# Performance work log

Measured on AMD Instinct MI355X. Metric: run time of the kernel, lower is better.

## Reference

```python
import jax, jax.numpy as jnp
import numpy as np


def conv3d(x, w, b, stride=(1, 1, 1)):
    # x: (B,C,D,H,W), w: (O,I,3,3,3), padding 1 on all three dims (PyTorch Conv3d k=3,p=1)
    y = jax.lax.conv_general_dilated(
        x, w, stride, [(1, 1)] * 3,
        dimension_numbers=("NCDHW", "OIDHW", "NCDHW"))
    return y + b[None, :, None, None, None]


def deconv3d(x, w, b):
    # ConvTranspose3d with k=3, s=1, p=1 == conv with spatially flipped kernel
    return conv3d(x, jnp.flip(w, axis=(2, 3, 4)), b)


def upsample2x(x):
    # nn.Upsample(scale_factor=(1,2,2), mode='nearest')
    return jnp.repeat(jnp.repeat(x, 2, axis=3), 2, axis=4)


def fo_pool(z, f, reverse):
    # linear gated recurrence h_t = f_t*h_{t-1} + (1-f_t)*z_t along band axis (dim 2)
    zt = jnp.moveaxis(z, 2, 0)
    ft = jnp.moveaxis(f, 2, 0)
    if reverse:
        zt, ft = zt[::-1], ft[::-1]

    def step(h, zf):
        zi, fi = zf
        h = fi * h + (1.0 - fi) * zi
        return h, h

    _, hs = jax.lax.scan(step, jnp.zeros_like(zt[0]), (zt, ft))
    if reverse:
        hs = hs[::-1]
    return jnp.moveaxis(hs, 0, 2)


def qrnn(gates, reverse):
    z, f = jnp.split(gates, 2, axis=1)
    return fo_pool(jnp.tanh(z), jax.nn.sigmoid(f), reverse)


def biqrnn(gates):
    z, f1, f2 = jnp.split(gates, 3, axis=1)
    z = jnp.tanh(z)
    return (fo_pool(z, jax.nn.sigmoid(f1), False)
            + fo_pool(z, jax.nn.sigmoid(f2), True))


def _forward(x, fe_w, fe_b, e0_w, e0_b, e1_w, e1_b, e2_w, e2_b, e3_w, e3_b,
             e4_w, e4_b, d0_w, d0_b, d1_w, d1_b, d2_w, d2_b, d3_w, d3_b,
             d4_w, d4_b, rec_w, rec_b):
    # feature extractor: BiQRNNConv3D(1 -> 16), gates 48ch
    fe = biqrnn(conv3d(x, fe_w, fe_b))                        # (B,16,31,256,256)
    # encoder (alternating direction: F,T,F,T,F)
    e0 = qrnn(conv3d(fe, e0_w, e0_b), False)                  # 16ch @256
    e1 = qrnn(conv3d(e0, e1_w, e1_b, stride=(1, 2, 2)), True) # 32ch @128
    e2 = qrnn(conv3d(e1, e2_w, e2_b), False)                  # 32ch @128
    e3 = qrnn(conv3d(e2, e3_w, e3_b, stride=(1, 2, 2)), True) # 64ch @64
    e4 = qrnn(conv3d(e3, e4_w, e4_b), False)                  # 64ch @64
    # decoder (reverse starts at True after encoder toggles)
    d0 = qrnn(deconv3d(e4, d0_w, d0_b), True)                 # 64ch @64
    d1 = qrnn(conv3d(upsample2x(d0 + e3), d1_w, d1_b), False) # 32ch @128
    d2 = qrnn(deconv3d(d1 + e2, d2_w, d2_b), True)            # 32ch @128
    d3 = qrnn(conv3d(upsample2x(d2 + e1), d3_w, d3_b), False) # 16ch @256
    d4 = qrnn(deconv3d(d3 + e0, d4_w, d4_b), True)            # 16ch @256
    out = d4 + fe
    # reconstructor: BiQRNNDeConv3D(16 -> 1), act='tanh'
    out = biqrnn(deconv3d(out, rec_w, rec_b))                 # (B,1,31,256,256)
    return out + x


def setup_inputs() -> dict:
    key = jax.random.key(0)
    ks = jax.random.split(key, 26)

    def W(k, o, i):
        return jax.random.normal(k, (o, i, 3, 3, 3), jnp.float32) * 0.05

    def Bv(k, o):
        return jax.random.normal(k, (o,), jnp.float32) * 0.01

    x = jax.random.normal(ks[0], (1, 1, 31, 256, 256), jnp.float32)
    inp = {"x": x}
    shapes = {
        "fe": (48, 1), "e0": (32, 16), "e1": (64, 16), "e2": (64, 32),
        "e3": (128, 32), "e4": (128, 64), "d0": (128, 64), "d1": (64, 64),
        "d2": (64, 32), "d3": (32, 32), "d4": (32, 16), "rec": (3, 16),
    }
    for j, (name, (o, i)) in enumerate(shapes.items()):
        inp[name + "_w"] = W(ks[1 + 2 * j], o, i)
        inp[name + "_b"] = Bv(ks[2 + 2 * j], o)
    return inp


def reference(x, fe_w, fe_b, e0_w, e0_b, e1_w, e1_b, e2_w, e2_b, e3_w, e3_b,
              e4_w, e4_b, d0_w, d0_b, d1_w, d1_b, d2_w, d2_b, d3_w, d3_b,
              d4_w, d4_b, rec_w, rec_b):
    return _forward(x, fe_w, fe_b, e0_w, e0_b, e1_w, e1_b, e2_w, e2_b,
                    e3_w, e3_b, e4_w, e4_b, d0_w, d0_b, d1_w, d1_b,
                    d2_w, d2_b, d3_w, d3_b, d4_w, d4_b, rec_w, rec_b)
```

## Files before the change

### kernel.cpp

```cpp
#include <hip/hip_runtime.h>
#include <hip/hip_bf16.h>
#include <cstdint>
#include <cstddef>

using f16 = _Float16;
typedef _Float16 f16x2 __attribute__((ext_vector_type(2)));
typedef _Float16 f16x8 __attribute__((ext_vector_type(8)));
typedef float f32x4 __attribute__((ext_vector_type(4)));

static constexpr int DD = 31;
static constexpr long long U  = 31LL * 256 * 256;
static constexpr long long V2 = 31LL * 128 * 128;
static constexpr long long POOL_UNITS = 56;
static constexpr int CP_CHUNK = 16;
static constexpr int COSPLIT_NONE = 1 << 30;

union U32H2 { unsigned u; f16x2 h; };

__device__ __forceinline__ float toF(float v) { return v; }
__device__ __forceinline__ float toF(f16 v) { return (float)v; }
__device__ __forceinline__ void stv(float* p, float v) { *p = v; }
__device__ __forceinline__ void stv(f16* p, float v) { *p = (f16)v; }
__device__ __forceinline__ float sigm(float x) { return 1.f / (1.f + __expf(-x)); }

// ... 24 lines not shown
    for (long long i = (long long)blockIdx.x * 256 + threadIdx.x; i < n; i += stride)
        p[i] = (f16)0.f;
}

__global__ __launch_bounds__(256)
void add_k(f16* __restrict__ a, const f16* __restrict__ b, long long n8)
{
    const long long i = (long long)blockIdx.x * 256 + threadIdx.x;
    if (i >= n8) return;
    uint4 va = ((const uint4*)a)[i];
    const uint4 vb = ((const uint4*)b)[i];
    va.x = addh2(va.x, vb.x); va.y = addh2(va.y, vb.y);
    va.z = addh2(va.z, vb.z); va.w = addh2(va.w, vb.w);
    ((uint4*)a)[i] = va;
}

__global__ __launch_bounds__(256)
void pack_w_k(const float* __restrict__ wt, f16* __restrict__ outp,
              int CIN, int nCo, int flip)
{
    const int e = blockIdx.x * 256 + threadIdx.x;
    const int nhg = (nCo + 7) >> 3;
    const int total = (CIN >> 3) * nhg * 9 * 64;
    if (e >= total) return;
    const int l = e & 63;
    const int r = e >> 6;
    const int r9 = r % 9;
    const int t2 = r / 9;
    const int hg = t2 % nhg;
    const int cc = t2 / nhg;
    const int kd = r9 / 3, Tg = r9 - kd * 3;
    const int n = hg * 8 + (l & 15);
    const int T = Tg * 4 + (l >> 4);
    f16x8 bv;
#pragma unroll
    for (int i = 0; i < 8; ++i) bv[i] = (f16)0.f;
    if (T <= 8 && n < nCo) {
        const int kh = T / 3, kw = T - (T / 3) * 3;
        const int st = flip ? ((2 - kd) * 9 + (2 - kh) * 3 + (2 - kw))
                            : (kd * 9 + kh * 3 + kw);
        const size_t wb8 = ((size_t)n * CIN + cc * 8) * 27 + st;
#pragma unroll
        for (int i = 0; i < 8; ++i)
            bv[i] = (f16)wt[wb8 + (size_t)i * 27];
    }
    *(f16x8*)(outp + (size_t)e * 8) = bv;
}

template<int STRIDE, bool FLIP, int CIN, int HOUT, int WOUT, int NT, bool PACKED,
         bool OUTIL>
__global__ __launch_bounds__(256)
void conv_mfma_k(const f16* __restrict__ in, const float* __restrict__ wt,
                 const f16x8* __restrict__ wb, const float* __restrict__ bias,
                 f16* __restrict__ out, f16* __restrict__ outF, int coSplit,
                 int nCo, int cg0, int nhg)
{
    constexpr int CIC = CIN / 8;
    constexpr int HIN = HOUT * STRIDE, WIN = WOUT * STRIDE;
    constexpr int WT = (WOUT > 128) ? 128 : WOUT;
    constexpr int RR = 128 / WT;
    constexpr int COLS = WOUT / WT;
    constexpr int TPD = (HOUT / RR) * COLS;
    constexpr int AH = STRIDE * (RR - 1) + 3;
    constexpr int AW = STRIDE * (WT - 1) + 3;
    constexpr int APOS = 3 * AH * AW;
    constexpr int NBENT = NT * 576;

    extern __shared__ unsigned lds[];
    unsigned* Alds = lds;
    unsigned* Blds = lds + APOS * 4;

    const int tid = threadIdx.x;
    const int l = tid & 63;
    const int wid = tid >> 6;

    const int bx = blockIdx.x;
    const int d0 = bx / TPD;
    const int rem = bx - d0 * TPD;
    const int h0 = (rem / COLS) * RR;
    const int wb_ = (rem % COLS) * WT;

    const int co_base = blockIdx.y * (16 * NT);
    const int nRem = nCo - co_base;
    const int hgBase = cg0 + blockIdx.y * (2 * NT);

    const int base_h = STRIDE * h0 - 1;
    const int base_w = STRIDE * wb_ - 1;
    constexpr size_t HWin = (size_t)HIN * WIN;
    constexpr size_t DHW = (size_t)DD * HWin;
    const unsigned* inu = (const unsigned*)in;

    int hho[2], wlo[2];
#pragma unroll
    for (int mt = 0; mt < 2; ++mt) {
        const int p = wid * 32 + mt * 16 + (l & 15);
        hho[mt] = p / WT;
        wlo[mt] = p - hho[mt] * WT;
    }
    const int g = l >> 4;
    int khg[3], kwg[3];
#pragma unroll
    for (int Tg = 0; Tg < 3; ++Tg) {
        int T = Tg * 4 + g;
        if (T > 8) T = 8;
        khg[Tg] = T / 3;
        kwg[Tg] = T - (T / 3) * 3;
    }
// ... 49 lines not shown
                const int T = Tg * 4 + gg;
                f16x8 bv;
                if (T <= 8 && n < nRem) {
                    const int kh = T / 3, kw = T - (T / 3) * 3;
                    const int st = FLIP ? ((2 - kd) * 9 + (2 - kh) * 3 + (2 - kw))
                                        : (kd * 9 + kh * 3 + kw);
                    const size_t wb8 = ((size_t)(co_base + n) * CIN + cc * 8) * 27 + st;
#pragma unroll
                    for (int e = 0; e < 8; ++e)
                        bv[e] = (f16)wt[wb8 + (size_t)e * 27];
                } else {
#pragma unroll
                    for (int e = 0; e < 8; ++e) bv[e] = (f16)0.f;
                }
                *(f16x8*)(Blds + (size_t)t * 4) = bv;
            }
        }
        __syncthreads();
#pragma unroll
        for (int kd = 0; kd < 3; ++kd) {
#pragma unroll
            for (int Tg = 0; Tg < 3; ++Tg) {
                f16x8 bfrag[NT];
#pragma unroll
                for (int nt = 0; nt < NT; ++nt)
                    bfrag[nt] = PACKED ? bfr[nt][kd * 3 + Tg]
                                       : *(const f16x8*)
                        (Blds + (size_t)(((nt * 9) + kd * 3 + Tg) * 64 + l) * 4);
                const int kh = khg[Tg], kw = kwg[Tg];
#pragma unroll
                for (int mt = 0; mt < 2; ++mt) {
                    const int hh = STRIDE * hho[mt] + kh;
                    const int ww = STRIDE * wlo[mt] + kw;
                    const f16x8 afrag = *(const f16x8*)
                        (Alds + (size_t)((kd * AH + hh) * AW + ww) * 4);
#pragma unroll
                    for (int nt = 0; nt < NT; ++nt)
                        acc[mt][nt] = __builtin_amdgcn_mfma_f32_16x16x32_f16(
                            afrag, bfrag[nt], acc[mt][nt], 0, 0, 0);
                }
            }
        }
    }

    const int n = l & 15;
#pragma unroll
    for (int nt = 0; nt < NT; ++nt) {
        const int ng = nt * 16 + n;
        if (ng < nRem) {
            const int co = co_base + ng;
            const float bv = bias[co];
            f16* dst = out;
            int cs = co;
            if (OUTIL && co >= coSplit) { dst = outF; cs = co - coSplit; }
#pragma unroll
            for (int mt = 0; mt < 2; ++mt) {
#pragma unroll
                for (int r = 0; r < 4; ++r) {
                    const int p = wid * 32 + mt * 16 + (l >> 4) * 4 + r;
                    const int hh = p / WT;
                    const int wl = p - hh * WT;
                    const int h = h0 + hh, w = wb_ + wl;
                    const float val = acc[mt][nt][r] + bv;
                    if (OUTIL) {
                        const size_t coPlane =
                            (size_t)(cs >> 1) * DD * HOUT * WOUT * 2 + (cs & 1);
                        dst[coPlane + ((size_t)d0 * HOUT + h) * WOUT * 2 +
                            (size_t)w * 2] = (f16)val;
                    } else {
                        out[((size_t)co * DD + d0) * HOUT * WOUT +
                            (size_t)h * WOUT + w] = (f16)val;
                    }
                }
            }
        }
    }
}

template<int CIN, int HLO, int WLO, int NT>
__global__ __launch_bounds__(256)
void conv_mfma_up_k(const f16* __restrict__ in, const f16x8* __restrict__ wb,
                    const float* __restrict__ bias, f16* __restrict__ out,
                    f16* __restrict__ outF, int coSplit,
                    int nCo, int cg0, int nhg)
{
    constexpr int CIC = CIN / 8;
    constexpr int HOUT = 2 * HLO, WOUT = 2 * WLO;
    constexpr int WT = (WOUT > 128) ? 128 : WOUT;
    constexpr int COLS = WOUT / WT;
    constexpr int TPD = HOUT * COLS;
    constexpr int AWLO = WT / 2 + 2;
    constexpr int AWLOP = AWLO + 1;
    constexpr int APOS = 3 * 2 * AWLO;

    extern __shared__ unsigned lds[];

    const int tid = threadIdx.x;
    const int l = tid & 63;
    const int wid = tid >> 6;

    const int bx = blockIdx.x;
    const int d0 = bx / TPD;
    const int rem = bx - d0 * TPD;
    const int h0 = rem / COLS;
    const int wb_ = (rem % COLS) * WT;

    const int co_base = blockIdx.y * (16 * NT);
    const int nRem = nCo - co_base;
    const int hgBase = cg0 + blockIdx.y * (2 * NT);

    const int rlo0 = (h0 - 1) >> 1;
    const int clo0 = (wb_ >> 1) - 1;

    constexpr size_t HWlo = (size_t)HLO * WLO;
    constexpr size_t DHW = (size_t)DD * HWlo;
    const unsigned* inu = (const unsigned*)in;

    int wpos[2];
#pragma unroll
    for (int mt = 0; mt < 2; ++mt)
        wpos[mt] = wid * 32 + mt * 16 + (l & 15);

    const int g = l >> 4;
    int khg[3], kwg[3];
#pragma unroll
    for (int Tg = 0; Tg < 3; ++Tg) {
        int T = Tg * 4 + g;
        if (T > 8) T = 8;
        khg[Tg] = T / 3;
        kwg[Tg] = T - (T / 3) * 3;
    }

    f32x4 acc[2][NT];
#pragma unroll
    for (int mt = 0; mt < 2; ++mt)
#pragma unroll
        for (int nt = 0; nt < NT; ++nt)
            acc[mt][nt] = (f32x4){0.f, 0.f, 0.f, 0.f};

    for (int cc = 0; cc < CIC; ++cc) {
        f16x8 bfr[NT][9];
#pragma unroll
        for (int nt = 0; nt < NT; ++nt)
#pragma unroll
            for (int r9 = 0; r9 < 9; ++r9)
                bfr[nt][r9] = wb[((size_t)cc * nhg + hgBase + nt * 2) * 9 * 64
                                 + (size_t)r9 * 64 + l];
        __syncthreads();
        for (int t = tid; t < APOS; t += 256) {
            const int ww = t % AWLO;
            const int t2 = t / AWLO;
            const int rr = t2 & 1;
            const int dd = t2 >> 1;
            const int d = d0 - 1 + dd;
            const int hlo = rlo0 + rr;
            const int wlo = clo0 + ww;
            uint4 val = make_uint4(0u, 0u, 0u, 0u);
            if ((unsigned)d < (unsigned)DD && (unsigned)hlo < (unsigned)HLO &&
                (unsigned)wlo < (unsigned)WLO) {
                const size_t gi = (size_t)(cc * 4) * DHW +
                                  (size_t)d * HWlo + (size_t)hlo * WLO + wlo;
                val.x = inu[gi];
                val.y = inu[gi + DHW];
                val.z = inu[gi + 2 * DHW];
                val.w = inu[gi + 3 * DHW];
            }
            *(uint4*)(lds + (size_t)((dd * 2 + rr) * AWLOP + ww) * 4) = val;
        }
        __syncthreads();
#pragma unroll
        for (int kd = 0; kd < 3; ++kd) {
#pragma unroll
            for (int Tg = 0; Tg < 3; ++Tg) {
                const int kh = khg[Tg], kw = kwg[Tg];
                const int rr = ((h0 + kh - 1) >> 1) - rlo0;
#pragma unroll
                for (int mt = 0; mt < 2; ++mt) {
                    const int iw = ((wpos[mt] + kw - 1) >> 1) + 1;
                    const f16x8 afrag = *(const f16x8*)
                        (lds + (size_t)((kd * 2 + rr) * AWLOP + iw) * 4);
#pragma unroll
                    for (int nt = 0; nt < NT; ++nt)
                        acc[mt][nt] = __builtin_amdgcn_mfma_f32_16x16x32_f16(
                            afrag, bfr[nt][kd * 3 + Tg], acc[mt][nt], 0, 0, 0);
                }
            }
        }
    }

    const int n = l & 15;
#pragma unroll
    for (int nt = 0; nt < NT; ++nt) {
        const int ng = nt * 16 + n;
        if (ng < nRem) {
            const int co = co_base + ng;
            const float bv = bias[co];
            f16* dst = out;
            int cs = co;
            if (co >= coSplit) { dst = outF; cs = co - coSplit; }
            const size_t coPlane = (size_t)(cs >> 1) * DD * HOUT * WOUT * 2 + (cs & 1);
#pragma unroll
            for (int mt = 0; mt < 2; ++mt) {
#pragma unroll
                for (int r = 0; r < 4; ++r) {
                    const int p = wid * 32 + mt * 16 + (l >> 4) * 4 + r;
                    dst[coPlane + ((size_t)d0 * HOUT + h0) * WOUT * 2 +
                        (size_t)(wb_ + p) * 2] = (f16)(acc[mt][nt][r] + bv);
                }
            }
        }
    }
}

template<int STRIDE, bool FLIP, int CO_BLK, bool OUT_IL>
__global__ __launch_bounds__(256, 2)
void conv3d_il_k(const f16* __restrict__ in, const float* __restrict__ wt,
                 const float* __restrict__ bias, f16* __restrict__ out,
                 int Cin, int Hin, int Win, int Hout, int Wout)
{
    extern __shared__ unsigned wl2[];
    const int co_base = blockIdx.y * CO_BLK;

    const int s8 = (blockIdx.x * 256 + threadIdx.x) * 8;
    const int w0 = s8 % Wout;
    const int sh = s8 / Wout;
    const int h0 = sh % Hout;
    const int d0 = sh / Hout;

    float acc[CO_BLK][8];
#pragma unroll
    for (int j = 0; j < CO_BLK; ++j) {
        const float bv = bias[co_base + j];
#pragma unroll
        for (int o = 0; o < 8; ++o) acc[j][o] = bv;
    }

    const size_t HWin = (size_t)Hin * Win;
    const int CP = Cin >> 1;

    for (int cp0 = 0; cp0 < CP; cp0 += CP_CHUNK) {
        const int cnp = (CP - cp0 < CP_CHUNK) ? (CP - cp0) : CP_CHUNK;
        __syncthreads();
        for (int t = threadIdx.x; t < cnp * 27 * CO_BLK; t += 256) {
            const int j = t % CO_BLK;
            const int k = (t / CO_BLK) % 27;
            const int cp = t / (CO_BLK * 27);
            int src;
            if (FLIP) {
                const int kd = k / 9, kh = (k / 3) % 3, kw = k % 3;
                src = (2 - kd) * 9 + (2 - kh) * 3 + (2 - kw);
            } else {
                src = k;
// ... 260 lines not shown
    const long long idx = (long long)blockIdx.x * 256 + threadIdx.x;
    if (idx >= (long long)C * HW) return;
    size_t base; size_t step;
    if (IL) {
        const long long pairIdx = idx / (2LL * HW);
        const int rem = (int)(idx - pairIdx * 2LL * HW);
        const int p = rem >> 1;
        const int par = rem & 1;
        base = ((size_t)pairIdx * DD * HW + p) * 2 + par;
        step = (size_t)HW * 2;
    } else {
        const int c = (int)(idx / HW);
        const int p = (int)(idx - (long long)c * HW);
        base = (size_t)c * DD * HW + p;
        step = (size_t)HW;
    }
    float h = 0.f;
    if (!reverse) {
        for (int d = 0; d < DD; ++d) {
            const size_t off = base + (size_t)d * step;
            const float zz = tanhf(toF(z[off]));
            const float ff = sigm(toF(f[off]));
            h = ff * h + (1.f - ff) * zz;
            float v = h;
            if (a1) v += toF(a1[off]);
            if (a2) v += toF(a2[off]);
            stv(out + off, v);
        }
    } else {
        for (int d = DD - 1; d >= 0; --d) {
            const size_t off = base + (size_t)d * step;
            const float zz = tanhf(toF(z[off]));
            const float ff = sigm(toF(f[off]));
            h = ff * h + (1.f - ff) * zz;
            float v = h;
            if (a1) v += toF(a1[off]);
            if (a2) v += toF(a2[off]);
            stv(out + off, v);
        }
    }
}

__global__ __launch_bounds__(256)
void diag_k(float* out, float v, int n)
{
    const int i = blockIdx.x * 256 + threadIdx.x;
    if (i < n) out[i] = v;
}


template<int STRIDE, bool FLIP, int CIN, int HOUT, int WOUT, int NT, bool PACKED,
         bool OUTIL>
static inline void mfma_launch(const f16* in, const float* w, const f16x8* wb,
                               const float* b, f16* out, f16* outF, int coSplit,
                               int co0, int nCo, int nhg, hipStream_t s)
{
    constexpr int WT = WOUT > 128 ? 128 : WOUT;
    constexpr int RR = 128 / WT;
    constexpr int AH = STRIDE * (RR - 1) + 3;
    constexpr int AW = STRIDE * (WT - 1) + 3;
    constexpr size_t lds = (size_t)(3 * AH * AW) * 16 +
                           (PACKED ? 0 : (size_t)NT * 9216);
    dim3 grid((unsigned)(DD * (HOUT / RR) * (WOUT / WT)),
              (unsigned)((nCo + 16 * NT - 1) / (16 * NT)));
    conv_mfma_k<STRIDE, FLIP, CIN, HOUT, WOUT, NT, PACKED, OUTIL>
        <<<grid, 256, lds, s>>>(
        in, w + (size_t)co0 * CIN * 27, wb, b + co0, out, outF, coSplit,
        nCo, co0 / 8, nhg);
}

template<int CIN, int HLO, int WLO, int NT>
static inline void mfma_up_launch(const f16* in, const f16x8* wb,
                                  const float* b, f16* out, f16* outF,
                                  int coSplit, int co0, int nCo,
                                  int nhg, hipStream_t s)
{
    constexpr int WOUT = 2 * WLO;
    constexpr int WT = WOUT > 128 ? 128 : WOUT;
    constexpr int AWLOP = WT / 2 + 3;
    constexpr size_t lds = (size_t)(3 * 2 * AWLOP) * 16;
    dim3 grid((unsigned)(DD * (2 * HLO) * (WOUT / WT)),
              (unsigned)((nCo + 16 * NT - 1) / (16 * NT)));
    conv_mfma_up_k<CIN, HLO, WLO, NT><<<grid, 256, lds, s>>>(
        in, wb, b + co0, out, outF, coSplit, nCo, co0 / 8, nhg);
}

static inline void conv_launch(const f16* in, const float* w, const float* b,
                               f16* out, int Cin, int co0, int nCo,
                               int Hin, int Win, int Hout, int Wout,
                               int stride, bool flip, hipStream_t s)
{
    const unsigned gx = (unsigned)((DD * (long long)Hout * Wout) / 2048);
    const float* wp = w + (size_t)co0 * Cin * 27;
    const float* bp = b + co0;
    const int cpc = (Cin / 2 < CP_CHUNK) ? Cin / 2 : CP_CHUNK;
    if (flip) {
        if (nCo % 4 == 0) {
            dim3 grid(gx, nCo / 4);
            conv3d_il_k<1, true, 4, true><<<grid, 256, (size_t)cpc * 27 * 4 * 4, s>>>(
                in, wp, bp, out, Cin, Hin, Win, Hout, Wout);
        } else {
            dim3 grid(gx, 1);
            conv3d_il_k<1, true, 3, false><<<grid, 256, (size_t)cpc * 27 * 3 * 4, s>>>(
                in, wp, bp, out, Cin, Hin, Win, Hout, Wout);
        }
    } else {
        dim3 grid(gx, nCo / 8);
        conv3d_il_k<1, false, 8, true><<<grid, 256, (size_t)cpc * 27 * 8 * 4, s>>>(
            in, wp, bp, out, Cin, Hin, Win, Hout, Wout);
    }
}

static inline void conv_up_launch(const f16* ia, const f16* ib, const float* w,
                                  const float* b, f16* out, int Cin, int co0,
                                  int nCo, int Hlo, int Wlo, hipStream_t s)
{
    const unsigned gx = (unsigned)((DD * 4LL * Hlo * Wlo) / 2048);
    const int cpc = (Cin / 2 < CP_CHUNK) ? Cin / 2 : CP_CHUNK;
    if (nCo % 8 == 0) {
        dim3 grid(gx, nCo / 8);
        conv3d_up_il_k<8><<<grid, 256, (size_t)cpc * 27 * 8 * 4, s>>>(
            ia, ib, w + (size_t)co0 * Cin * 27, b + co0, out, Cin, Hlo, Wlo);
    } else {
        dim3 grid(gx, nCo / 4);
        conv3d_up_il_k<4><<<grid, 256, (size_t)cpc * 27 * 4 * 4, s>>>(
            ia, ib, w + (size_t)co0 * Cin * 27, b + co0, out, Cin, Hlo, Wlo);
    }
}

template<bool IL, typename TA1, typename TA2, typename TO>
static inline void pool_launch(const f16* z, const f16* f, TO* o, const TA1* a1,
                               const TA2* a2, int C, int HW, int rev,
                               hipStream_t s)
{
    const long long tot = (long long)C * HW;
    fo_pool_k<IL, TA1, TA2, TO><<<(unsigned)((tot + 255) / 256), 256, 0, s>>>(
        z, f, o, a1, a2, C, HW, rev);
}

static inline void pack_launch(const float* w, f16* outp, int CIN, int nCo,
                               int flip, hipStream_t s)
{
    const int total = (CIN / 8) * ((nCo + 7) / 8) * 9 * 64;
    pack_w_k<<<(total + 255) / 256, 256, 0, s>>>(w, outp, CIN, nCo, flip);
}

static inline void add_launch(f16* a, const f16* b, long long n, hipStream_t s)
{
    const long long n8 = n / 8;
    add_k<<<(unsigned)((n8 + 255) / 256), 256, 0, s>>>(a, b, n8);
}

static constexpr size_t pk_sz(int CIN, int nCo)
{ return (size_t)(CIN / 8) * ((nCo + 7) / 8) * 9 * 64 * 8; }

static void run_net(const float* x, const float* const* W, const float* const* B,
                    float* out, f16* P, bool packed, hipStream_t s)
{
    const f16* np = nullptr;
    const float* npf = nullptr;

    f16* WP = P + 56 * U;
    f16* PK_e0 = WP;
    f16* PK_e1 = PK_e0 + pk_sz(16, 32);
    f16* PK_e2 = PK_e1 + pk_sz(16, 64);
    f16* PK_e3 = PK_e2 + pk_sz(32, 64);
    f16* PK_e4 = PK_e3 + pk_sz(32, 128);
    f16* PK_d0 = PK_e4 + pk_sz(64, 128);
    f16* PK_d2 = PK_d0 + pk_sz(64, 128);
    f16* PK_d1 = PK_d0;
    f16* PK_d3 = PK_d1 + pk_sz(64, 64);
    f16* PK_d4 = PK_d3 + pk_sz(32, 32);
    f16* PK_rec = PK_d4 + pk_sz(16, 32);
    if (packed) {
        pack_launch(W[1], PK_e0, 16, 32, 0, s);
        pack_launch(W[2], PK_e1, 16, 64, 0, s);
        pack_launch(W[3], PK_e2, 32, 64, 0, s);
        pack_launch(W[4], PK_e3, 32, 128, 0, s);
        pack_launch(W[5], PK_e4, 64, 128, 0, s);
        pack_launch(W[6], PK_d0, 64, 128, 1, s);
        pack_launch(W[8], PK_d2, 32, 64, 1, s);
    }

#define MFMA_CALL(S, F, CI, H, Wd, NTv, in_, wt_, wb_, bi_, out_, co0_, nco_, nhg_) \
    do { if (packed) mfma_launch<S, F, CI, H, Wd, NTv, true, true>(in_, wt_, (const f16x8*)(wb_), bi_, out_, nullptr, COSPLIT_NONE, co0_, nco_, nhg_, s); \
         else        mfma_launch<S, F, CI, H, Wd, NTv, false, true>(in_, wt_, nullptr, bi_, out_, nullptr, COSPLIT_NONE, co0_, nco_, nhg_, s); } while (0)

    fill_k<<<2048, 256, 0, s>>>(P, POOL_UNITS * U);

    f16* FE = P + 32 * U;
    for (int a = 0; a < 16; a += 4) {
        conv_fe_k<<<992, 256, 0, s>>>(x, W[0] + (size_t)a * 27,        B[0] + a,      P);
        conv_fe_k<<<992, 256, 0, s>>>(x, W[0] + (size_t)(16 + a) * 27, B[0] + 16 + a, P + 4 * U);
        conv_fe_k<<<992, 256, 0, s>>>(x, W[0] + (size_t)(32 + a) * 27, B[0] + 32 + a, P + 8 * U);
        pool_launch<true, f16, float, f16>(P, P + 4 * U, P + 12 * U, np, npf, 4, 65536, 0, s);
        pool_launch<true, f16, float, f16>(P, P + 8 * U, FE + (size_t)a * U, P + 12 * U, npf, 4, 65536, 1, s);
    }

    f16* E0 = P + 16 * U;
    if (packed) {
        f16* G = P + 48 * U;
        mfma_launch<1, false, 16, 256, 256, 2, true, true>(
            FE, W[1], (const f16x8*)PK_e0, B[1], P, G, 16, 0, 24, 4, s);
        pool_launch<true, f16, float, f16>(P, G, E0, np, npf, 8, 65536, 0, s);
        mfma_launch<1, false, 16, 256, 256, 1, true, true>(
            FE, W[1], (const f16x8*)PK_e0, B[1], G, nullptr, COSPLIT_NONE,
            24, 8, 4, s);
        pool_launch<true, f16, float, f16>(P + 8 * U, G, E0 + 8 * U, np, npf, 8, 65536, 0, s);
    } else {
        MFMA_CALL(1, false, 16, 256, 256, 1, FE, W[1], PK_e0, B[1], P, 0, 16, 4);
        for (int a = 0; a < 16; a += 8) {
            f16* G = P + 48 * U;
            MFMA_CALL(1, false, 16, 256, 256, 1, FE, W[1], PK_e0, B[1], G, 16 + a, 8, 4);
            pool_launch<true, f16, float, f16>(P + (size_t)a * U, G, E0 + (size_t)a * U,
                                               np, npf, 8, 65536, 0, s);
        }
    }

    f16* E1 = P;
    {
        f16* G = P + 32 * U;
        MFMA_CALL(2, false, 16, 128, 128, 2, E0, W[2], PK_e1, B[2], G, 0, 64, 8);
        pool_launch<true, f16, float, f16>(G, G + 8 * U, E1, np, npf, 32, 16384, 1, s);
    }

    f16* E2 = P + 8 * U;
    {
        f16* G = P + 32 * U;
        MFMA_CALL(1, false, 32, 128, 128, 2, E1, W[3], PK_e2, B[3], G, 0, 64, 8);
        pool_launch<true, f16, float, f16>(G, G + 8 * U, E2, np, npf, 32, 16384, 0, s);
    }

    f16* E3 = P + 32 * U;
    {
        f16* G = P + 48 * U;
        MFMA_CALL(2, false, 32, 64, 64, 2, E2, W[4], PK_e3, B[4], G, 0, 128, 16);
        pool_launch<true, f16, float, f16>(G, G + 4 * U, E3, np, npf, 64, 4096, 1, s);
    }

    f16* E4 = P + 40 * U;
    {
        f16* G = P + 48 * U;
        MFMA_CALL(1, false, 64, 64, 64, 2, E3, W[5], PK_e4, B[5], G, 0, 128, 16);
        pool_launch<true, f16, float, f16>(G, G + 4 * U, E4, np, npf, 64, 4096, 0, s);
    }

    f16* D0 = P + 44 * U;
    {
        f16* G = P + 48 * U;
        MFMA_CALL(1, true, 64, 64, 64, 2, E4, W[6], PK_d0, B[6], G, 0, 128, 16);
        pool_launch<true, f16, float, f16>(G, G + 4 * U, D0, np, npf, 64, 4096, 1, s);
    }
    if (packed) {
        pack_launch(W[7],  PK_d1, 64, 64, 0, s);
        pack_launch(W[9],  PK_d3, 32, 32, 0, s);
        pack_launch(W[10], PK_d4, 16, 32, 1, s);
        pack_launch(W[11], PK_rec, 16, 3, 1, s);
    }

    f16* D1 = P + 36 * U;
    if (packed)
        add_launch(D0, E3, 4 * U, s);
    for (int a = 0; a < 32; a += 16) {
        f16* G = P + 48 * U;
        if (packed) {
            mfma_up_launch<64, 64, 64, 1>(D0, (const f16x8*)PK_d1, B[7], G,
                                          nullptr, COSPLIT_NONE, a, 16, 8, s);
            mfma_up_launch<64, 64, 64, 1>(D0, (const f16x8*)PK_d1, B[7], G + 4 * U,
                                          nullptr, COSPLIT_NONE, 32 + a, 16, 8, s);
        } else {
            conv_up_launch(D0, E3, W[7], B[7], G,         64, a,      16, 64, 64, s);
            conv_up_launch(D0, E3, W[7], B[7], G + 4 * U, 64, 32 + a, 16, 64, 64, s);
        }
        pool_launch<true, f16, float, f16>(G, G + 4 * U, D1 + (size_t)a * V2,
                                           E2 + (size_t)a * V2, npf, 16, 16384, 0, s);
    }

    f16* D2 = P + 8 * U;
    for (int a = 0; a < 32; a += 16) {
        f16* G = P + 48 * U;
        MFMA_CALL(1, true, 32, 128, 128, 1, D1, W[8], PK_d2, B[8], G,         a,      16, 8);
        MFMA_CALL(1, true, 32, 128, 128, 1, D1, W[8], PK_d2, B[8], G + 4 * U, 32 + a, 16, 8);
        pool_launch<true, f16, float, f16>(G, G + 4 * U, D2 + (size_t)a * V2, np, npf, 16, 16384, 1, s);
    }

    f16* D3 = P + 32 * U;
    if (packed) {
        f16* G = P + 48 * U;
        add_launch(D2, E1, 8 * U, s);
        mfma_up_launch<32, 128, 128, 2>(D2, (const f16x8*)PK_d3, B[9], D3,
                                        G, 16, 0, 24, 4, s);
        pool_launch<true, f16, float, f16>(D3, G, D3, E0, npf, 8, 65536, 0, s);
        mfma_up_launch<32, 128, 128, 1>(D2, (const f16x8*)PK_d3, B[9], G,
                                        nullptr, COSPLIT_NONE, 24, 8, 4, s);
        pool_launch<true, f16, float, f16>(D3 + 8 * U, G, D3 + 8 * U,
                                           E0 + 8 * U, npf, 8, 65536, 0, s);
    } else {
        for (int a = 0; a < 16; a += 4) {
            f16* G = P + 48 * U;
            conv_up_launch(D2, E1, W[9], B[9], G,         32, a,      4, 128, 128, s);
            conv_up_launch(D2, E1, W[9], B[9], G + 4 * U, 32, 16 + a, 4, 128, 128, s);
            pool_launch<true, f16, float, f16>(G, G + 4 * U, D3 + (size_t)a * U,
                                               E0 + (size_t)a * U, npf, 4, 65536, 0, s);
        }
    }

    f16* FE2 = P;
    for (int a = 0; a < 16; a += 4) {
        f16* G = P + 16 * U;
        conv_fe_k<<<992, 256, 0, s>>>(x, W[0] + (size_t)a * 27,        B[0] + a,      G);
        conv_fe_k<<<992, 256, 0, s>>>(x, W[0] + (size_t)(16 + a) * 27, B[0] + 16 + a, G + 4 * U);
        conv_fe_k<<<992, 256, 0, s>>>(x, W[0] + (size_t)(32 + a) * 27, B[0] + 32 + a, G + 8 * U);
        pool_launch<true, f16, float, f16>(G, G + 4 * U, G + 12 * U, np, npf, 4, 65536, 0, s);
        pool_launch<true, f16, float, f16>(G, G + 8 * U, FE2 + (size_t)a * U, G + 12 * U, npf, 4, 65536, 1, s);
    }

    f16* D4 = P + 16 * U;
    if (packed) {
        f16* G = P + 48 * U;
        mfma_launch<1, true, 16, 256, 256, 2, true, true>(
            D3, W[10], (const f16x8*)PK_d4, B[10], D4, G, 16, 0, 24, 4, s);
        pool_launch<true, f16, float, f16>(D4, G, D4, FE2, npf, 8, 65536, 1, s);
        mfma_launch<1, true, 16, 256, 256, 1, true, true>(
            D3, W[10], (const f16x8*)PK_d4, B[10], G, nullptr, COSPLIT_NONE,
            24, 8, 4, s);
        pool_launch<true, f16, float, f16>(D4 + 8 * U, G, D4 + 8 * U,
                                           FE2 + 8 * U, npf, 8, 65536, 1, s);
    } else {
        for (int a = 0; a < 16; a += 4) {
            f16* G = P + 48 * U;
            conv_launch(D3, W[10], B[10], G,         16, a,      4, 256, 256, 256, 256, 1, true, s);
            conv_launch(D3, W[10], B[10], G + 4 * U, 16, 16 + a, 4, 256, 256, 256, 256, 1, true, s);
            pool_launch<true, f16, float, f16>(G, G + 4 * U, D4 + (size_t)a * U,
                                               FE2 + (size_t)a * U, npf, 4, 65536, 1, s);
        }
    }

    {
        f16* G = P + 32 * U;
        f16* TMP = P + 35 * U;
        if (packed) {
            mfma_launch<1, true, 16, 256, 256, 1, true, false>(
                D4, W[11], (const f16x8*)PK_rec, B[11], G, nullptr, COSPLIT_NONE,
                0, 3, 1, s);
        } else {
            conv_launch(D4, W[11], B[11], G, 16, 0, 3, 256, 256, 256, 256, 1, true, s);
        }
        pool_launch<false, f16, float, f16>(G, G + 1 * U, TMP, np, npf, 1, 65536, 0, s);
        pool_launch<false, f16, float, float>(G, G + 2 * U, out, TMP, x, 1, 65536, 1, s);
    }
#undef MFMA_CALL
}

extern "C" void kernel_launch(void* const* d_in, const int* in_sizes, int n_in,
                              void* d_out, int out_size, void* d_ws, size_t ws_size,
                              hipStream_t stream)
{
    const float* x = (const float*)d_in[0];
    const float* W[12];
    const float* B[12];
    for (int i = 0; i < 12; ++i) {
        W[i] = (const float*)d_in[1 + 2 * i];
        B[i] = (const float*)d_in[2 + 2 * i];
    }

    const size_t need_base = (size_t)(POOL_UNITS * U) * sizeof(f16);
    const size_t need_pack = (size_t)(57 * U) * sizeof(f16);
    if (ws_size >= need_pack) {
        run_net(x, W, B, (float*)d_out, (f16*)d_ws, true, stream);
    } else if (ws_size >= need_base) {
        run_net(x, W, B, (float*)d_out, (f16*)d_ws, false, stream);
    } else {
        const float ws_mb = (float)((double)ws_size / 1048576.0);
        diag_k<<<(out_size + 255) / 256, 256, 0, stream>>>(
            (float*)d_out, ws_mb, out_size);
    }
}
```

Baseline: 4.282 ms.

## Stage upsampled input in LDS at full resolution and merge d1 conv launches

The upsample-conv kernel now writes the nearest-upsampled input tile into LDS at output resolution (WT+2 columns), duplicating each low-res pixel. A-fragment reads then become a contiguous index wpos+kw with no shift arithmetic, and neighbouring lanes hit distinct addresses instead of duplicated ones. The d1 stage uses NT=2 with two 32-channel launches writing z directly into D1, followed by a single in-place pool, replacing four launches and two pools. The cost is roughly twice the LDS footprint and global-load work per tile, plus higher register pressure from NT=2.

```diff
diff --git a/kernel.cpp b/kernel.cpp
--- a/kernel.cpp
+++ b/kernel.cpp
@@ -293,9 +293,8 @@
     constexpr int WT = (WOUT > 128) ? 128 : WOUT;
     constexpr int COLS = WOUT / WT;
     constexpr int TPD = HOUT * COLS;
-    constexpr int AWLO = WT / 2 + 2;
-    constexpr int AWLOP = AWLO + 1;
-    constexpr int APOS = 3 * 2 * AWLO;
+    constexpr int AWHI = WT + 2;
+    constexpr int APOS = 3 * 2 * AWHI;
 
     extern __shared__ unsigned lds[];
 
@@ -314,7 +313,6 @@
     const int hgBase = cg0 + blockIdx.y * (2 * NT);
 
     const int rlo0 = (h0 - 1) >> 1;
-    const int clo0 = (wb_ >> 1) - 1;
 
     constexpr size_t HWlo = (size_t)HLO * WLO;
     constexpr size_t DHW = (size_t)DD * HWlo;
@@ -352,13 +350,13 @@
                                  + (size_t)r9 * 64 + l];
         __syncthreads();
         for (int t = tid; t < APOS; t += 256) {
-            const int ww = t % AWLO;
-            const int t2 = t / AWLO;
+            const int ww = t % AWHI;
+            const int t2 = t / AWHI;
             const int rr = t2 & 1;
             const int dd = t2 >> 1;
             const int d = d0 - 1 + dd;
             const int hlo = rlo0 + rr;
-            const int wlo = clo0 + ww;
+            const int wlo = (wb_ - 1 + ww) >> 1;
             uint4 val = make_uint4(0u, 0u, 0u, 0u);
             if ((unsigned)d < (unsigned)DD && (unsigned)hlo < (unsigned)HLO &&
                 (unsigned)wlo < (unsigned)WLO) {
@@ -369,7 +367,7 @@
                 val.z = inu[gi + 2 * DHW];
                 val.w = inu[gi + 3 * DHW];
             }
-            *(uint4*)(lds + (size_t)((dd * 2 + rr) * AWLOP + ww) * 4) = val;
+            *(uint4*)(lds + (size_t)((dd * 2 + rr) * AWHI + ww) * 4) = val;
         }
         __syncthreads();
 #pragma unroll
@@ -380,9 +378,9 @@
                 const int rr = ((h0 + kh - 1) >> 1) - rlo0;
 #pragma unroll
                 for (int mt = 0; mt < 2; ++mt) {
-                    const int iw = ((wpos[mt] + kw - 1) >> 1) + 1;
+                    const int iw = wpos[mt] + kw;
                     const f16x8 afrag = *(const f16x8*)
-                        (lds + (size_t)((kd * 2 + rr) * AWLOP + iw) * 4);
+                        (lds + (size_t)((kd * 2 + rr) * AWHI + iw) * 4);
 #pragma unroll
                     for (int nt = 0; nt < NT; ++nt)
                         acc[mt][nt] = __builtin_amdgcn_mfma_f32_16x16x32_f16(
@@ -793,8 +791,8 @@
 {
     constexpr int WOUT = 2 * WLO;
     constexpr int WT = WOUT > 128 ? 128 : WOUT;
-    constexpr int AWLOP = WT / 2 + 3;
-    constexpr size_t lds = (size_t)(3 * 2 * AWLOP) * 16;
+    constexpr int AWHI = WT + 2;
+    constexpr size_t lds = (size_t)(3 * 2 * AWHI) * 16;
     dim3 grid((unsigned)(DD * (2 * HLO) * (WOUT / WT)),
               (unsigned)((nCo + 16 * NT - 1) / (16 * NT)));
     conv_mfma_up_k<CIN, HLO, WLO, NT><<<grid, 256, lds, s>>>(
@@ -975,21 +973,22 @@
     }
 
     f16* D1 = P + 36 * U;
-    if (packed)
+    if (packed) {
+        f16* G = P + 48 * U;
         add_launch(D0, E3, 4 * U, s);
-    for (int a = 0; a < 32; a += 16) {
-        f16* G = P + 48 * U;
-        if (packed) {
-            mfma_up_launch<64, 64, 64, 1>(D0, (const f16x8*)PK_d1, B[7], G,
-                                          nullptr, COSPLIT_NONE, a, 16, 8, s);
-            mfma_up_launch<64, 64, 64, 1>(D0, (const f16x8*)PK_d1, B[7], G + 4 * U,
-                                          nullptr, COSPLIT_NONE, 32 + a, 16, 8, s);
-        } else {
+        mfma_up_launch<64, 64, 64, 2>(D0, (const f16x8*)PK_d1, B[7], D1,
+                                      nullptr, COSPLIT_NONE, 0, 32, 8, s);
+        mfma_up_launch<64, 64, 64, 2>(D0, (const f16x8*)PK_d1, B[7], G,
+                                      nullptr, COSPLIT_NONE, 32, 32, 8, s);
+        pool_launch<true, f16, float, f16>(D1, G, D1, E2, npf, 32, 16384, 0, s);
+    } else {
+        for (int a = 0; a < 32; a += 16) {
+            f16* G = P + 48 * U;
             conv_up_launch(D0, E3, W[7], B[7], G,         64, a,      16, 64, 64, s);
             conv_up_launch(D0, E3, W[7], B[7], G + 4 * U, 64, 32 + a, 16, 64, 64, s);
-        }
-        pool_launch<true, f16, float, f16>(G, G + 4 * U, D1 + (size_t)a * V2,
-                                           E2 + (size_t)a * V2, npf, 16, 16384, 0, s);
+            pool_launch<true, f16, float, f16>(G, G + 4 * U, D1 + (size_t)a * V2,
+                                               E2 + (size_t)a * V2, npf, 16, 16384, 0, s);
+        }
     }
 
     f16* D2 = P + 8 * U;
```

Measured after the change: 4.302 ms. About the same (+0.5%).

## Keep feature-extractor output in spare workspace and merge decoder channel-chunk launches

Applied to the files above, without the earlier changes.

When the workspace is large enough, the feature-extractor output is written to a dedicated region past the packed weights. The decoder then reuses it instead of recomputing the conv and bidirectional pool a second time. The d1 and d2 stages also drop their two-iteration channel loops in favour of one wider launch per gate half (NT=2, 32 channels) with a single pool over all channels, cutting launch count. In exchange the workspace must hold more memory, and the whole saving depends on the harness providing that space.

```diff
diff --git a/kernel.cpp b/kernel.cpp
--- a/kernel.cpp
+++ b/kernel.cpp
@@ -871,7 +871,7 @@
 { return (size_t)(CIN / 8) * ((nCo + 7) / 8) * 9 * 64 * 8; }
 
 static void run_net(const float* x, const float* const* W, const float* const* B,
-                    float* out, f16* P, bool packed, hipStream_t s)
+                    float* out, f16* P, bool packed, bool saveFE, hipStream_t s)
 {
     const f16* np = nullptr;
     const float* npf = nullptr;
@@ -904,7 +904,7 @@
 
     fill_k<<<2048, 256, 0, s>>>(P, POOL_UNITS * U);
 
-    f16* FE = P + 32 * U;
+    f16* FE = saveFE ? (P + 57 * U) : (P + 32 * U);
     for (int a = 0; a < 16; a += 4) {
         conv_fe_k<<<992, 256, 0, s>>>(x, W[0] + (size_t)a * 27,        B[0] + a,      P);
         conv_fe_k<<<992, 256, 0, s>>>(x, W[0] + (size_t)(16 + a) * 27, B[0] + 16 + a, P + 4 * U);
@@ -975,29 +975,37 @@
     }
 
     f16* D1 = P + 36 * U;
-    if (packed)
+    if (packed) {
+        f16* G = P + 48 * U;
         add_launch(D0, E3, 4 * U, s);
-    for (int a = 0; a < 32; a += 16) {
-        f16* G = P + 48 * U;
-        if (packed) {
-            mfma_up_launch<64, 64, 64, 1>(D0, (const f16x8*)PK_d1, B[7], G,
-                                          nullptr, COSPLIT_NONE, a, 16, 8, s);
-            mfma_up_launch<64, 64, 64, 1>(D0, (const f16x8*)PK_d1, B[7], G + 4 * U,
-                                          nullptr, COSPLIT_NONE, 32 + a, 16, 8, s);
-        } else {
+        mfma_up_launch<64, 64, 64, 2>(D0, (const f16x8*)PK_d1, B[7], D1,
+                                      nullptr, COSPLIT_NONE, 0, 32, 8, s);
+        mfma_up_launch<64, 64, 64, 2>(D0, (const f16x8*)PK_d1, B[7], G,
+                                      nullptr, COSPLIT_NONE, 32, 32, 8, s);
+        pool_launch<true, f16, float, f16>(D1, G, D1, E2, npf, 32, 16384, 0, s);
+    } else {
+        for (int a = 0; a < 32; a += 16) {
+            f16* G = P + 48 * U;
             conv_up_launch(D0, E3, W[7], B[7], G,         64, a,      16, 64, 64, s);
             conv_up_launch(D0, E3, W[7], B[7], G + 4 * U, 64, 32 + a, 16, 64, 64, s);
-        }
-        pool_launch<true, f16, float, f16>(G, G + 4 * U, D1 + (size_t)a * V2,
-                                           E2 + (size_t)a * V2, npf, 16, 16384, 0, s);
+            pool_launch<true, f16, float, f16>(G, G + 4 * U, D1 + (size_t)a * V2,
+                                               E2 + (size_t)a * V2, npf, 16, 16384, 0, s);
+        }
     }
 
     f16* D2 = P + 8 * U;
-    for (int a = 0; a < 32; a += 16) {
+    if (packed) {
         f16* G = P + 48 * U;
-        MFMA_CALL(1, true, 32, 128, 128, 1, D1, W[8], PK_d2, B[8], G,         a,      16, 8);
-        MFMA_CALL(1, true, 32, 128, 128, 1, D1, W[8], PK_d2, B[8], G + 4 * U, 32 + a, 16, 8);
-        pool_launch<true, f16, float, f16>(G, G + 4 * U, D2 + (size_t)a * V2, np, npf, 16, 16384, 1, s);
+        MFMA_CALL(1, true, 32, 128, 128, 2, D1, W[8], PK_d2, B[8], D2, 0, 32, 8);
+        MFMA_CALL(1, true, 32, 128, 128, 2, D1, W[8], PK_d2, B[8], G, 32, 32, 8);
+        pool_launch<true, f16, float, f16>(D2, G, D2, np, npf, 32, 16384, 1, s);
+    } else {
+        for (int a = 0; a < 32; a += 16) {
+            f16* G = P + 48 * U;
+            MFMA_CALL(1, true, 32, 128, 128, 1, D1, W[8], PK_d2, B[8], G,         a,      16, 8);
+            MFMA_CALL(1, true, 32, 128, 128, 1, D1, W[8], PK_d2, B[8], G + 4 * U, 32 + a, 16, 8);
+            pool_launch<true, f16, float, f16>(G, G + 4 * U, D2 + (size_t)a * V2, np, npf, 16, 16384, 1, s);
+        }
     }
 
     f16* D3 = P + 32 * U;
@@ -1021,14 +1029,19 @@
         }
     }
 
-    f16* FE2 = P;
-    for (int a = 0; a < 16; a += 4) {
-        f16* G = P + 16 * U;
-        conv_fe_k<<<992, 256, 0, s>>>(x, W[0] + (size_t)a * 27,        B[0] + a,      G);
-        conv_fe_k<<<992, 256, 0, s>>>(x, W[0] + (size_t)(16 + a) * 27, B[0] + 16 + a, G + 4 * U);
-        conv_fe_k<<<992, 256, 0, s>>>(x, W[0] + (size_t)(32 + a) * 27, B[0] + 32 + a, G + 8 * U);
-        pool_launch<true, f16, float, f16>(G, G + 4 * U, G + 12 * U, np, npf, 4, 65536, 0, s);
-        pool_launch<true, f16, float, f16>(G, G + 8 * U, FE2 + (size_t)a * U, G + 12 * U, npf, 4, 65536, 1, s);
+    f16* FE2;
+    if (saveFE) {
+        FE2 = FE;
+    } else {
+        FE2 = P;
+        for (int a = 0; a < 16; a += 4) {
+            f16* G = P + 16 * U;
+            conv_fe_k<<<992, 256, 0, s>>>(x, W[0] + (size_t)a * 27,        B[0] + a,      G);
+            conv_fe_k<<<992, 256, 0, s>>>(x, W[0] + (size_t)(16 + a) * 27, B[0] + 16 + a, G + 4 * U);
+            conv_fe_k<<<992, 256, 0, s>>>(x, W[0] + (size_t)(32 + a) * 27, B[0] + 32 + a, G + 8 * U);
+            pool_launch<true, f16, float, f16>(G, G + 4 * U, G + 12 * U, np, npf, 4, 65536, 0, s);
+            pool_launch<true, f16, float, f16>(G, G + 8 * U, FE2 + (size_t)a * U, G + 12 * U, npf, 4, 65536, 1, s);
+        }
     }
 
     f16* D4 = P + 16 * U;
@@ -1082,10 +1095,12 @@
 
     const size_t need_base = (size_t)(POOL_UNITS * U) * sizeof(f16);
     const size_t need_pack = (size_t)(57 * U) * sizeof(f16);
+    const size_t need_save = (size_t)(74 * U) * sizeof(f16);
     if (ws_size >= need_pack) {
-        run_net(x, W, B, (float*)d_out, (f16*)d_ws, true, stream);
+        const bool saveFE = (ws_size >= need_save);
+        run_net(x, W, B, (float*)d_out, (f16*)d_ws, true, saveFE, stream);
     } else if (ws_size >= need_base) {
-        run_net(x, W, B, (float*)d_out, (f16*)d_ws, false, stream);
+        run_net(x, W, B, (float*)d_out, (f16*)d_ws, false, false, stream);
     } else {
         const float ws_mb = (float)((double)ws_size / 1048576.0);
         diag_k<<<(out_size + 255) / 256, 256, 0, stream>>>(
```

Result: faster. 4.040 ms (-5.7%).

## Merge split conv launches into single wide-NT launches with dual output split

Applied to the files above, without the earlier changes.

Adds a second output pointer and split threshold to the MFMA conv kernels so one launch can write its z/f gate channels to separate buffers. Several layers (e0, d1, d2, d3) that were split into multiple conv+pool launches are merged into one conv launch followed by one pool launch. The channel tile NT rises from 2 to 4 for the 128- and 64-resolution layers, so each block covers more output channels and reuses its staged input more. The costs are more accumulator registers per thread, possibly lower occupancy, and larger scratch buffers live at once.

```diff
diff --git a/kernel.cpp b/kernel.cpp
--- a/kernel.cpp
+++ b/kernel.cpp
@@ -100,7 +100,8 @@
 __global__ __launch_bounds__(256)
 void conv_mfma_k(const f16* __restrict__ in, const float* __restrict__ wt,
                  const f16x8* __restrict__ wb, const float* __restrict__ bias,
-                 f16* __restrict__ out, f16* __restrict__ outF, int coSplit,
+                 f16* __restrict__ out, f16* __restrict__ outF,
+                 f16* __restrict__ outF2, int coSplit, int coSplit2,
                  int nCo, int cg0, int nhg)
 {
     constexpr int CIC = CIN / 8;
@@ -256,7 +257,8 @@
             const float bv = bias[co];
             f16* dst = out;
             int cs = co;
-            if (OUTIL && co >= coSplit) { dst = outF; cs = co - coSplit; }
+            if (OUTIL && co >= coSplit2) { dst = outF2; cs = co - coSplit2; }
+            else if (OUTIL && co >= coSplit) { dst = outF; cs = co - coSplit; }
 #pragma unroll
             for (int mt = 0; mt < 2; ++mt) {
 #pragma unroll
@@ -285,8 +287,8 @@
 __global__ __launch_bounds__(256)
 void conv_mfma_up_k(const f16* __restrict__ in, const f16x8* __restrict__ wb,
                     const float* __restrict__ bias, f16* __restrict__ out,
-                    f16* __restrict__ outF, int coSplit,
-                    int nCo, int cg0, int nhg)
+                    f16* __restrict__ outF, f16* __restrict__ outF2,
+                    int coSplit, int coSplit2, int nCo, int cg0, int nhg)
 {
     constexpr int CIC = CIN / 8;
     constexpr int HOUT = 2 * HLO, WOUT = 2 * WLO;
@@ -401,7 +403,8 @@
             const float bv = bias[co];
             f16* dst = out;
             int cs = co;
-            if (co >= coSplit) { dst = outF; cs = co - coSplit; }
+            if (co >= coSplit2) { dst = outF2; cs = co - coSplit2; }
+            else if (co >= coSplit) { dst = outF; cs = co - coSplit; }
             const size_t coPlane = (size_t)(cs >> 1) * DD * HOUT * WOUT * 2 + (cs & 1);
 #pragma unroll
             for (int mt = 0; mt < 2; ++mt) {
@@ -768,7 +771,8 @@
 template<int STRIDE, bool FLIP, int CIN, int HOUT, int WOUT, int NT, bool PACKED,
          bool OUTIL>
 static inline void mfma_launch(const f16* in, const float* w, const f16x8* wb,
-                               const float* b, f16* out, f16* outF, int coSplit,
+                               const float* b, f16* out, f16* outF, f16* outF2,
+                               int coSplit, int coSplit2,
                                int co0, int nCo, int nhg, hipStream_t s)
 {
     constexpr int WT = WOUT > 128 ? 128 : WOUT;
@@ -781,15 +785,15 @@
               (unsigned)((nCo + 16 * NT - 1) / (16 * NT)));
     conv_mfma_k<STRIDE, FLIP, CIN, HOUT, WOUT, NT, PACKED, OUTIL>
         <<<grid, 256, lds, s>>>(
-        in, w + (size_t)co0 * CIN * 27, wb, b + co0, out, outF, coSplit,
-        nCo, co0 / 8, nhg);
+        in, w + (size_t)co0 * CIN * 27, wb, b + co0, out, outF, outF2,
+        coSplit, coSplit2, nCo, co0 / 8, nhg);
 }
 
 template<int CIN, int HLO, int WLO, int NT>
 static inline void mfma_up_launch(const f16* in, const f16x8* wb,
                                   const float* b, f16* out, f16* outF,
-                                  int coSplit, int co0, int nCo,
-                                  int nhg, hipStream_t s)
+                                  f16* outF2, int coSplit, int coSplit2,
+                                  int co0, int nCo, int nhg, hipStream_t s)
 {
     constexpr int WOUT = 2 * WLO;
     constexpr int WT = WOUT > 128 ? 128 : WOUT;
@@ -798,7 +802,7 @@
     dim3 grid((unsigned)(DD * (2 * HLO) * (WOUT / WT)),
               (unsigned)((nCo + 16 * NT - 1) / (16 * NT)));
     conv_mfma_up_k<CIN, HLO, WLO, NT><<<grid, 256, lds, s>>>(
-        in, wb, b + co0, out, outF, coSplit, nCo, co0 / 8, nhg);
+        in, wb, b + co0, out, outF, outF2, coSplit, coSplit2, nCo, co0 / 8, nhg);
 }
 
 static inline void conv_launch(const f16* in, const float* w, const float* b,
@@ -875,6 +879,7 @@
 {
     const f16* np = nullptr;
     const float* npf = nullptr;
+    f16* NPF16 = nullptr;
 
     f16* WP = P + 56 * U;
     f16* PK_e0 = WP;
@@ -899,8 +904,8 @@
     }
 
 #define MFMA_CALL(S, F, CI, H, Wd, NTv, in_, wt_, wb_, bi_, out_, co0_, nco_, nhg_) \
-    do { if (packed) mfma_launch<S, F, CI, H, Wd, NTv, true, true>(in_, wt_, (const f16x8*)(wb_), bi_, out_, nullptr, COSPLIT_NONE, co0_, nco_, nhg_, s); \
-         else        mfma_launch<S, F, CI, H, Wd, NTv, false, true>(in_, wt_, nullptr, bi_, out_, nullptr, COSPLIT_NONE, co0_, nco_, nhg_, s); } while (0)
+    do { if (packed) mfma_launch<S, F, CI, H, Wd, NTv, true, true>(in_, wt_, (const f16x8*)(wb_), bi_, out_, NPF16, NPF16, COSPLIT_NONE, COSPLIT_NONE, co0_, nco_, nhg_, s); \
+         else        mfma_launch<S, F, CI, H, Wd, NTv, false, true>(in_, wt_, nullptr, bi_, out_, NPF16, NPF16, COSPLIT_NONE, COSPLIT_NONE, co0_, nco_, nhg_, s); } while (0)
 
     fill_k<<<2048, 256, 0, s>>>(P, POOL_UNITS * U);
 
@@ -915,14 +920,10 @@
 
     f16* E0 = P + 16 * U;
     if (packed) {
-        f16* G = P + 48 * U;
         mfma_launch<1, false, 16, 256, 256, 2, true, true>(
-            FE, W[1], (const f16x8*)PK_e0, B[1], P, G, 16, 0, 24, 4, s);
-        pool_launch<true, f16, float, f16>(P, G, E0, np, npf, 8, 65536, 0, s);
-        mfma_launch<1, false, 16, 256, 256, 1, true, true>(
-            FE, W[1], (const f16x8*)PK_e0, B[1], G, nullptr, COSPLIT_NONE,
-            24, 8, 4, s);
-        pool_launch<true, f16, float, f16>(P + 8 * U, G, E0 + 8 * U, np, npf, 8, 65536, 0, s);
+            FE, W[1], (const f16x8*)PK_e0, B[1], P, E0, NPF16,
+            16, COSPLIT_NONE, 0, 32, 4, s);
+        pool_launch<true, f16, float, f16>(P, E0, E0, np, npf, 16, 65536, 0, s);
     } else {
         MFMA_CALL(1, false, 16, 256, 256, 1, FE, W[1], PK_e0, B[1], P, 0, 16, 4);
         for (int a = 0; a < 16; a += 8) {
@@ -936,35 +937,35 @@
     f16* E1 = P;
     {
         f16* G = P + 32 * U;
-        MFMA_CALL(2, false, 16, 128, 128, 2, E0, W[2], PK_e1, B[2], G, 0, 64, 8);
+        MFMA_CALL(2, false, 16, 128, 128, 4, E0, W[2], PK_e1, B[2], G, 0, 64, 8);
         pool_launch<true, f16, float, f16>(G, G + 8 * U, E1, np, npf, 32, 16384, 1, s);
     }
 
     f16* E2 = P + 8 * U;
     {
         f16* G = P + 32 * U;
-        MFMA_CALL(1, false, 32, 128, 128, 2, E1, W[3], PK_e2, B[3], G, 0, 64, 8);
+        MFMA_CALL(1, false, 32, 128, 128, 4, E1, W[3], PK_e2, B[3], G, 0, 64, 8);
         pool_launch<true, f16, float, f16>(G, G + 8 * U, E2, np, npf, 32, 16384, 0, s);
     }
 
     f16* E3 = P + 32 * U;
     {
         f16* G = P + 48 * U;
-        MFMA_CALL(2, false, 32, 64, 64, 2, E2, W[4], PK_e3, B[4], G, 0, 128, 16);
+        MFMA_CALL(2, false, 32, 64, 64, 4, E2, W[4], PK_e3, B[4], G, 0, 128, 16);
         pool_launch<true, f16, float, f16>(G, G + 4 * U, E3, np, npf, 64, 4096, 1, s);
     }
 
     f16* E4 = P + 40 * U;
     {
         f16* G = P + 48 * U;
-        MFMA_CALL(1, false, 64, 64, 64, 2, E3, W[5], PK_e4, B[5], G, 0, 128, 16);
+        MFMA_CALL(1, false, 64, 64, 64, 4, E3, W[5], PK_e4, B[5], G, 0, 128, 16);
         pool_launch<true, f16, float, f16>(G, G + 4 * U, E4, np, npf, 64, 4096, 0, s);
     }
 
     f16* D0 = P + 44 * U;
     {
         f16* G = P + 48 * U;
-        MFMA_CALL(1, true, 64, 64, 64, 2, E4, W[6], PK_d0, B[6], G, 0, 128, 16);
+        MFMA_CALL(1, true, 64, 64, 64, 4, E4, W[6], PK_d0, B[6], G, 0, 128, 16);
         pool_launch<true, f16, float, f16>(G, G + 4 * U, D0, np, npf, 64, 4096, 1, s);
     }
     if (packed) {
@@ -975,29 +976,38 @@
     }
 
     f16* D1 = P + 36 * U;
-    if (packed)
+    if (packed) {
+        f16* G = P + 48 * U;
         add_launch(D0, E3, 4 * U, s);
-    for (int a = 0; a < 32; a += 16) {
-        f16* G = P + 48 * U;
-        if (packed) {
-            mfma_up_launch<64, 64, 64, 1>(D0, (const f16x8*)PK_d1, B[7], G,
-                                          nullptr, COSPLIT_NONE, a, 16, 8, s);
-            mfma_up_launch<64, 64, 64, 1>(D0, (const f16x8*)PK_d1, B[7], G + 4 * U,
-                                          nullptr, COSPLIT_NONE, 32 + a, 16, 8, s);
-        } else {
+        mfma_up_launch<64, 64, 64, 4>(D0, (const f16x8*)PK_d1, B[7], D1,
+                                      G, NPF16, 32, COSPLIT_NONE, 0, 64, 8, s);
+        pool_launch<true, f16, float, f16>(D1, G, D1, E2, npf, 32, 16384, 0, s);
+    } else {
+        for (int a = 0; a < 32; a += 16) {
+            f16* G = P + 48 * U;
             conv_up_launch(D0, E3, W[7], B[7], G,         64, a,      16, 64, 64, s);
             conv_up_launch(D0, E3, W[7], B[7], G + 4 * U, 64, 32 + a, 16, 64, 64, s);
-        }
-        pool_launch<true, f16, float, f16>(G, G + 4 * U, D1 + (size_t)a * V2,
-                                           E2 + (size_t)a * V2, npf, 16, 16384, 0, s);
+            pool_launch<true, f16, float, f16>(G, G + 4 * U, D1 + (size_t)a * V2,
+                                               E2 + (size_t)a * V2, npf, 16, 16384, 0, s);
+        }
     }
 
     f16* D2 = P + 8 * U;
-    for (int a = 0; a < 32; a += 16) {
+    if (packed) {
         f16* G = P + 48 * U;
-        MFMA_CALL(1, true, 32, 128, 128, 1, D1, W[8], PK_d2, B[8], G,         a,      16, 8);
-        MFMA_CALL(1, true, 32, 128, 128, 1, D1, W[8], PK_d2, B[8], G + 4 * U, 32 + a, 16, 8);
-        pool_launch<true, f16, float, f16>(G, G + 4 * U, D2 + (size_t)a * V2, np, npf, 16, 16384, 1, s);
+        if (true) {
+            if (packed) mfma_launch<1, true, 32, 128, 128, 4, true, true>(
+                D1, W[8], (const f16x8*)PK_d2, B[8], D2, G, NPF16,
+                32, COSPLIT_NONE, 0, 64, 8, s);
+        }
+        pool_launch<true, f16, float, f16>(D2, G, D2, np, npf, 32, 16384, 1, s);
+    } else {
+        for (int a = 0; a < 32; a += 16) {
+            f16* G = P + 48 * U;
+            MFMA_CALL(1, true, 32, 128, 128, 1, D1, W[8], PK_d2, B[8], G,         a,      16, 8);
+            MFMA_CALL(1, true, 32, 128, 128, 1, D1, W[8], PK_d2, B[8], G + 4 * U, 32 + a, 16, 8);
+            pool_launch<true, f16, float, f16>(G, G + 4 * U, D2 + (size_t)a * V2, np, npf, 16, 16384, 1, s);
+        }
     }
 
     f16* D3 = P + 32 * U;
@@ -1005,10 +1015,8 @@
         f16* G = P + 48 * U;
         add_launch(D2, E1, 8 * U, s);
         mfma_up_launch<32, 128, 128, 2>(D2, (const f16x8*)PK_d3, B[9], D3,
-                                        G, 16, 0, 24, 4, s);
-        pool_launch<true, f16, float, f16>(D3, G, D3, E0, npf, 8, 65536, 0, s);
-        mfma_up_launch<32, 128, 128, 1>(D2, (const f16x8*)PK_d3, B[9], G,
-                                        nullptr, COSPLIT_NONE, 24, 8, 4, s);
+                                        P, G, 16, 24, 0, 32, 4, s);
+        pool_launch<true, f16, float, f16>(D3, P, D3, E0, npf, 8, 65536, 0, s);
         pool_launch<true, f16, float, f16>(D3 + 8 * U, G, D3 + 8 * U,
                                            E0 + 8 * U, npf, 8, 65536, 0, s);
     } else {
@@ -1035,11 +1043,12 @@
     if (packed) {
         f16* G = P + 48 * U;
         mfma_launch<1, true, 16, 256, 256, 2, true, true>(
-            D3, W[10], (const f16x8*)PK_d4, B[10], D4, G, 16, 0, 24, 4, s);
+            D3, W[10], (const f16x8*)PK_d4, B[10], D4, G, NPF16,
+            16, COSPLIT_NONE, 0, 24, 4, s);
         pool_launch<true, f16, float, f16>(D4, G, D4, FE2, npf, 8, 65536, 1, s);
         mfma_launch<1, true, 16, 256, 256, 1, true, true>(
-            D3, W[10], (const f16x8*)PK_d4, B[10], G, nullptr, COSPLIT_NONE,
-            24, 8, 4, s);
+            D3, W[10], (const f16x8*)PK_d4, B[10], G, NPF16, NPF16,
+            COSPLIT_NONE, COSPLIT_NONE, 24, 8, 4, s);
         pool_launch<true, f16, float, f16>(D4 + 8 * U, G, D4 + 8 * U,
                                            FE2 + 8 * U, npf, 8, 65536, 1, s);
     } else {
@@ -1057,8 +1066,8 @@
         f16* TMP = P + 35 * U;
         if (packed) {
             mfma_launch<1, true, 16, 256, 256, 1, true, false>(
-                D4, W[11], (const f16x8*)PK_rec, B[11], G, nullptr, COSPLIT_NONE,
-                0, 3, 1, s);
+                D4, W[11], (const f16x8*)PK_rec, B[11], G, NPF16, NPF16,
+                COSPLIT_NONE, COSPLIT_NONE, 0, 3, 1, s);
         } else {
             conv_launch(D4, W[11], B[11], G, 16, 0, 3, 256, 256, 256, 256, 1, true, s);
         }
```

After: 3.730 ms. 1.15x faster.
